# Kernel optimization log

Measured on AMD Instinct MI355X. Metric: run time of the kernel, lower is better.

Reference implementation:

```python
import jax, jax.numpy as jnp
import numpy as np

D_MODEL = 256
GAMMA = 0.9          # ret_D is built in the torch forward but never applied to the output; kept for fidelity notes
SCALE_BASE = 512     # XPOS default
TEMP = 10000.0
TWO_PI = 2.0 * np.pi


def sine_pos_embed(x):
    """DETR-style 1D sine position embedding with an all-ones mask (as in forward).
    x: [B,T,C] -> pos: [1,T,C] (mask is [1,T] ones, so batch dim broadcasts)."""
    T, C = x.shape[1], x.shape[2]
    x_embed = jnp.arange(1, T + 1, dtype=jnp.float32)          # cumsum of ones
    x_embed = x_embed / (x_embed[-1] + 1e-6) * TWO_PI          # normalize=True
    dim_t = TEMP ** (2.0 * (jnp.arange(C) // 2).astype(jnp.float32) / C)
    pos = x_embed[:, None] / dim_t                             # [T,C]
    pos = jnp.stack([jnp.sin(pos[:, 0::2]), jnp.cos(pos[:, 1::2])], axis=2).reshape(T, C)
    return pos[None].astype(x.dtype)


def _dup_interleave(m):
    # [L, d/2] -> [L, d], columns repeated pairwise: [a,b] -> [a,a,b,b]
    return jnp.repeat(m, 2, axis=-1)


def _rotate_every_two(x):
    x1, x2 = x[..., 0::2], x[..., 1::2]
    return jnp.stack([-x2, x1], axis=-1).reshape(x.shape)


def xpos_apply(x, downscale=False):
    """RetNet XPOS rotary embedding. x: [B,L,d]."""
    L, d = x.shape[1], x.shape[2]
    half = d // 2
    scale_vec = (jnp.arange(0, d, 2, dtype=jnp.float32) + 0.4 * d) / (1.4 * d)   # [d/2]
    power = jnp.arange(L, dtype=jnp.float32) / SCALE_BASE
    scale = scale_vec[None, :] ** power[:, None]                                  # [L, d/2]
    inv_freq = 1.0 / (TEMP ** (jnp.arange(half, dtype=jnp.float32) / half))
    sinusoid = jnp.arange(L, dtype=jnp.float32)[:, None] * inv_freq[None, :]      # [L, d/2]
    sin, cos = jnp.sin(sinusoid), jnp.cos(sinusoid)
    if downscale:
        scale = 1.0 / scale
    sin_s = _dup_interleave(sin * scale)[None].astype(x.dtype)   # [1,L,d]
    cos_s = _dup_interleave(cos * scale)[None].astype(x.dtype)
    return x * cos_s + _rotate_every_two(x) * sin_s


def setup_inputs() -> dict:
    key = jax.random.key(0)
    ks = jax.random.split(key, 8)
    B, TXT, VID, D = 16, 32, 2048, D_MODEL
    S = TXT + VID
    inp = {
        "src": jax.random.normal(ks[0], (B, S, D), dtype=jnp.float32),
        "learn_vid_ret": jax.random.normal(ks[1], (VID * VID, 1), dtype=jnp.float32),
        "W_txt_Q": jax.random.normal(ks[2], (D, D), dtype=jnp.float32) / D,
        "W_txt_K": jax.random.normal(ks[3], (D, D), dtype=jnp.float32) / D,
        "W_txt_V": jax.random.normal(ks[4], (D, D), dtype=jnp.float32) / D,
        "W_vid_Q": jax.random.normal(ks[5], (D, D), dtype=jnp.float32) / D,
        "W_vid_K": jax.random.normal(ks[6], (D, D), dtype=jnp.float32) / D,
        "W_vid_V": jax.random.normal(ks[7], (D, D), dtype=jnp.float32) / D,
        "txt_length": TXT,
    }
    return inp


def reference(src, learn_vid_ret, W_txt_Q, W_txt_K, W_txt_V, W_vid_Q, W_vid_K, W_vid_V, txt_length):
    S = src.shape[1]
    vid_length = S - txt_length

    # learned retention mask over the video block
    learn_ret = jax.nn.sigmoid(learn_vid_ret.reshape(vid_length, vid_length))
    diag = jnp.eye(vid_length, dtype=src.dtype)
    video_ret = (1.0 - diag) * learn_ret
    loss_sparsity = jnp.mean(jnp.abs(video_ret))

    # full [S,S] mask: ones everywhere, sigmoid(learned) on the vid-vid block
    ret_mask = jnp.ones((S, S), dtype=src.dtype).at[txt_length:, txt_length:].set(learn_ret)

    txt_mem = src[:, :txt_length]   # [B,TXT,D]
    vid_mem = src[:, txt_length:]   # [B,VID,D]

    pos = sine_pos_embed(txt_mem)   # [1,TXT,D]
    txt_Q = (pos + txt_mem) @ W_txt_Q
    txt_K = (pos + txt_mem) @ W_txt_K
    vid_Q = xpos_apply(vid_mem @ W_vid_Q)
    vid_K = xpos_apply(vid_mem @ W_vid_K, downscale=True)

    Q = jnp.concatenate([txt_Q, vid_Q], axis=1)                  # [B,S,D]
    K = jnp.concatenate([txt_K, vid_K], axis=1)                  # [B,S,D]
    V = jnp.concatenate([txt_mem @ W_txt_V, vid_mem @ W_vid_V], axis=1)

    # retention: QK^T elementwise-masked (no softmax), then weighted V sum
    scores = jnp.einsum('bsd,btd->bst', Q, K) * ret_mask[None]   # [B,S,S]
    out = scores @ V                                             # [B,S,D]
    return out, loss_sparsity
```

## Files before the change

kernel.cpp:

```cpp
#include <hip/hip_runtime.h>

#define B_   16
#define TXT  32
#define VID  2048
#define D_   256
#define S_   2080
#define SP   2176
#define NKT  34
#define GTOT 17424

typedef unsigned short ushort_t;
typedef __attribute__((ext_vector_type(8))) short short8;
typedef __attribute__((ext_vector_type(4))) short short4v;
typedef __attribute__((ext_vector_type(4))) float f32x4;
typedef __attribute__((ext_vector_type(16))) float f32x16;

__device__ __forceinline__ ushort_t f2bf(float f) {
  unsigned u = __builtin_bit_cast(unsigned, f);
  unsigned r = (u + 0x7FFFu + ((u >> 16) & 1u)) >> 16;
  return (ushort_t)r;
}
__device__ __forceinline__ float bf2f(ushort_t h) {
  unsigned u = ((unsigned)h) << 16;
  return __builtin_bit_cast(float, u);
}

__device__ __forceinline__ void g2l16(void* lds, const void* g) {
  __builtin_amdgcn_global_load_lds(
      (const __attribute__((address_space(1))) char*)g,
      (__attribute__((address_space(3))) char*)lds, 16, 0, 0);
}

__device__ __forceinline__ f32x4 mfma16(short8 a, short8 b, f32x4 c) {
  return __builtin_amdgcn_mfma_f32_16x16x32_bf16(a, b, c, 0, 0, 0);
}
__device__ __forceinline__ f32x16 mfma32(short8 a, short8 b, f32x16 c) {
  return __builtin_amdgcn_mfma_f32_32x32x16_bf16(a, b, c, 0, 0, 0);
}


__global__ void tbl_kernel(float* __restrict__ tbl) {
  int idx = blockIdx.x * 256 + threadIdx.x;
  int n = idx >> 7, i = idx & 127;
  float invf = powf(10000.0f, -(float)i / 128.0f);
  float ang = (float)n * invf;
  float s, co;
  sincosf(ang, &s, &co);
  float sv = ((float)(2 * i) + 102.4f) / 358.4f;
  float sc = powf(sv, (float)n / 512.0f);
  float4 r;
  r.x = co * sc; r.y = s * sc; r.z = co / sc; r.w = s / sc;
  *(float4*)(tbl + (size_t)idx * 4) = r;
}

__global__ void sig_loss_kernel(const float* __restrict__ learn, ushort_t* __restrict__ sigp,
                                float* __restrict__ loss) {
  const int tid = threadIdx.x;
  const int base = (blockIdx.x * 256 + tid) * 8;
  float4 v0 = *(const float4*)(learn + base);
  float4 v1 = *(const float4*)(learn + base + 4);
  float vals[8] = {v0.x, v0.y, v0.z, v0.w, v1.x, v1.y, v1.z, v1.w};
  float acc = 0.f;
  short8 sh;
  #pragma unroll
  for (int j = 0; j < 8; ++j) {
    int idx = base + j;
    float s = 1.0f / (1.0f + expf(-vals[j]));
    sh[j] = (short)f2bf(s);
    int rr = idx >> 11, cc = idx & 2047;
    if (rr != cc) acc += s;
  }
  *(short8*)(sigp + base) = sh;
  __shared__ float red[256];
  red[tid] = acc;
  __syncthreads();
  #pragma unroll
  for (int st = 128; st > 0; st >>= 1) {
    if (tid < st) red[tid] += red[tid + st];
    __syncthreads();
  }
  if (tid == 0) atomicAdd(loss, red[0] * (1.0f / 4194304.0f));
}

__global__ void cvt_kernel(const float* __restrict__ src, ushort_t* __restrict__ srcb) {
  int i = blockIdx.x * 256 + threadIdx.x;
  int b = i >> 16;
  int rem = i & 65535;
  int row = rem >> 5, c8 = (rem & 31) * 8;
  const float* p = src + ((size_t)b * S_ + TXT + row) * D_ + c8;
  float4 v0 = *(const float4*)p;
  float4 v1 = *(const float4*)(p + 4);
  short8 h;
  h[0] = (short)f2bf(v0.x); h[1] = (short)f2bf(v0.y); h[2] = (short)f2bf(v0.z); h[3] = (short)f2bf(v0.w);
  h[4] = (short)f2bf(v1.x); h[5] = (short)f2bf(v1.y); h[6] = (short)f2bf(v1.z); h[7] = (short)f2bf(v1.w);
  *(short8*)(srcb + ((size_t)b * VID + row) * D_ + c8) = h;
}

__global__ void pad0_kernel(ushort_t* __restrict__ Qp, ushort_t* __restrict__ Ks,
                            ushort_t* __restrict__ VTs) {
  int i = blockIdx.x * 256 + threadIdx.x;
  short8 z = {0, 0, 0, 0, 0, 0, 0, 0};
  if (i < 49152) {
    int bb = i / 3072, rem = i - bb * 3072;
    int row = 2080 + (rem >> 5), c8 = (rem & 31) * 8;
    *(short8*)(Qp + ((size_t)bb * SP + row) * D_ + c8) = z;
  } else if (i < 65536) {
    int j = i - 49152; int bb = j >> 10; int rem = j & 1023;
    int kstep = rem >> 6, ch = rem & 63;
    size_t base = ((size_t)(bb * NKT + 32)) << 14;
    *(short8*)(Ks + base + kstep * 1024 + 512 + ch * 8) = z;
  } else if (i < 81920) {
    int j = i - 65536; int bb = j >> 10; int rem = j & 1023;
    size_t base = (((size_t)(bb * NKT + 32)) << 14) + 8192;
    *(short8*)(VTs + base + rem * 8) = z;
  }
}

__global__ void wt_kernel(const float* __restrict__ Wq, const float* __restrict__ Wk,
                          const float* __restrict__ Wv, ushort_t* __restrict__ WT) {
  __shared__ float t[64][68];
  const int k0 = blockIdx.x * 64, n0 = blockIdx.y * 64, mt = blockIdx.z;
  const float* W = (mt == 0) ? Wq : (mt == 1) ? Wk : Wv;
  int tid = threadIdx.x;
  int r = tid >> 4, cq = (tid & 15) * 4;
  #pragma unroll
  for (int m = 0; m < 4; ++m) {
    int k = m * 16 + r;
    float4 v = *(const float4*)(W + (size_t)(k0 + k) * 256 + n0 + cq);
    t[k][cq] = v.x; t[k][cq + 1] = v.y; t[k][cq + 2] = v.z; t[k][cq + 3] = v.w;
  }
  __syncthreads();
  #pragma unroll
  for (int m = 0; m < 4; ++m) {
    int n = m * 16 + r;
    short4v h;
    h[0] = (short)f2bf(t[cq + 0][n]);
    h[1] = (short)f2bf(t[cq + 1][n]);
    h[2] = (short)f2bf(t[cq + 2][n]);
    h[3] = (short)f2bf(t[cq + 3][n]);
    *(short4v*)(WT + ((size_t)mt * D_ + n0 + n) * D_ + k0 + cq) = h;
  }
}

__global__ void txt_kernel(const float* __restrict__ src,
                           const float* __restrict__ Wq, const float* __restrict__ Wk,
                           const float* __restrict__ Wv,
                           ushort_t* __restrict__ Qp, ushort_t* __restrict__ Ks,
                           ushort_t* __restrict__ VTs) {
  __shared__ float a_s[8][256];
  __shared__ float x_s[8][256];
  const int tg = blockIdx.x;
  const int b  = blockIdx.y;
  const int c  = threadIdx.x;
  #pragma unroll
  for (int t = 0; t < 8; ++t) {
    int row = tg * 8 + t;
    float x = src[((size_t)b * S_ + row) * D_ + c];
    float xe = (float)(row + 1) * (6.283185307179586f / (32.0f + 1e-6f));
    int i = c >> 1;
    float dimt = powf(10000.0f, (2.0f * (float)i) / 256.0f);
    float ang = xe / dimt;
    float pv = (c & 1) ? cosf(ang) : sinf(ang);
    x_s[t][c] = x;
    a_s[t][c] = x + pv;
  }
  __syncthreads();
  float q[8] = {0,0,0,0,0,0,0,0}, k[8] = {0,0,0,0,0,0,0,0}, v[8] = {0,0,0,0,0,0,0,0};
  for (int kk = 0; kk < 256; ++kk) {
    float wq = Wq[(size_t)kk * 256 + c];
    float wk = Wk[(size_t)kk * 256 + c];
    float wv = Wv[(size_t)kk * 256 + c];
    #pragma unroll
    for (int t = 0; t < 8; ++t) {
      q[t] = fmaf(a_s[t][kk], wq, q[t]);
      k[t] = fmaf(a_s[t][kk], wk, k[t]);
      v[t] = fmaf(x_s[t][kk], wv, v[t]);
    }
  }
  #pragma unroll
  for (int t = 0; t < 8; ++t) {
    int row = tg * 8 + t;
    Qp[((size_t)b * SP + row) * D_ + c] = f2bf(q[t]);
    size_t kidx = ((((size_t)(b * NKT)) << 14) + (c >> 4) * 1024 + row * 16 + (c & 15)) ^ (((row >> 2) & 1) << 3);
    Ks[kidx] = f2bf(k[t]);
    size_t vidx = ((((size_t)(b * NKT)) << 14) + (row >> 4) * 4096 + c * 16 + (row & 15)) ^ (((c >> 2) & 1) << 3);
    VTs[vidx] = f2bf(v[t]);
  }
}

template <int MODE>
__global__ __launch_bounds__(256, 2) void vid_gemm(
    const float* __restrict__ src, const ushort_t* __restrict__ srcb,
    const ushort_t* __restrict__ WT, const float* __restrict__ tbl,
    ushort_t* __restrict__ Qp, ushort_t* __restrict__ Ks, ushort_t* __restrict__ VTs) {
  __shared__ __align__(16) ushort_t ldsA[64 * 64];
  __shared__ __align__(16) ushort_t ldsB[64 * 64];

  const int rt = blockIdx.x;
  const int b  = blockIdx.y;
  const int ct = blockIdx.z;
  const int nt = ct >> 2;
  const int n0 = (ct & 3) * 64;
  const int tid = threadIdx.x;
  const int wv = tid >> 6, lane = tid & 63, l15 = lane & 15, l4 = lane >> 4;

  f32x4 acc[4];
  #pragma unroll
  for (int t2 = 0; t2 < 4; ++t2) { acc[t2][0] = 0.f; acc[t2][1] = 0.f; acc[t2][2] = 0.f; acc[t2][3] = 0.f; }

  for (int kk = 0; kk < 256; kk += 64) {
    if (MODE == 1) {
      #pragma unroll
      for (int m = 0; m < 2; ++m) {
        int p = (m * 256 + tid) * 16;
        int r = p >> 7;
        int cb = (p & 127) ^ ((r & 7) << 4);
        g2l16((char*)ldsA + p,
              (const char*)(srcb + ((size_t)b * VID + rt * 64 + r) * D_ + kk) + cb);
      }
    } else {
      #pragma unroll
      for (int m = 0; m < 4; ++m) {
        int q = m * 256 + tid;
        int r = q >> 4;
        int kc = (q & 15) * 4;
        const float4 v = *(const float4*)(src + ((size_t)b * S_ + TXT + rt * 64 + r) * D_ + kk + kc);
        short4v h;
        h[0] = (short)f2bf(v.x); h[1] = (short)f2bf(v.y);
        h[2] = (short)f2bf(v.z); h[3] = (short)f2bf(v.w);
        int off = ((r << 7) + (kc << 1)) ^ ((r & 7) << 4);
        *(short4v*)((char*)ldsA + off) = h;
      }
    }
    #pragma unroll
    for (int m = 0; m < 2; ++m) {
      int p = (m * 256 + tid) * 16;
      int nl = p >> 7;
      int c = (p & 127) ^ ((nl & 7) << 4);
      g2l16((char*)ldsB + p, (const char*)(WT + ((size_t)nt * D_ + n0 + nl) * D_ + kk) + c);
    }
    __syncthreads();
    #pragma unroll
    for (int ks = 0; ks < 2; ++ks) {
      int ar = wv * 16 + l15;
      int aoff = ((ar << 7) + ((ks * 32 + l4 * 8) << 1)) ^ ((ar & 7) << 4);
      short8 av = *(const short8*)((const char*)ldsA + aoff);
      #pragma unroll
      for (int t2 = 0; t2 < 4; ++t2) {
        int nl = t2 * 16 + l15;
        int boff = ((nl << 7) + ((ks * 32 + l4 * 8) << 1)) ^ ((nl & 7) << 4);
        short8 bv = *(const short8*)((const char*)ldsB + boff);
        acc[t2] = mfma16(av, bv, acc[t2]);
      }
    }
    __syncthreads();
  }

  const int rowl = wv * 16 + l4 * 4;
  if (nt < 2) {
    #pragma unroll
    for (int t2 = 0; t2 < 4; ++t2) {
      int c = n0 + t2 * 16 + l15;
      #pragma unroll
      for (int r = 0; r < 4; ++r) {
        int n = rt * 64 + rowl + r;
        float x = acc[t2][r];
        float xp = __shfl_xor(x, 1);
        const float4 tb = *(const float4*)(tbl + ((size_t)n * 128 + (c >> 1)) * 4);
        float cs = (nt == 0) ? tb.x : tb.z;
        float ss = (nt == 0) ? tb.y : tb.w;
        float val = (c & 1) ? fmaf(x, cs, xp * ss) : fmaf(x, cs, -xp * ss);
        if (nt == 0) {
          Qp[((size_t)b * SP + TXT + n) * D_ + c] = f2bf(val);
        } else {
          int kvg = TXT + n;
          size_t kidx = ((((size_t)(b * NKT + (kvg >> 6))) << 14) + (c >> 4) * 1024 + (kvg & 63) * 16 + (c & 15))
                        ^ (((kvg >> 2) & 1) << 3);
          Ks[kidx] = f2bf(val);
        }
      }
    }
  } else {
    #pragma unroll
    for (int t2 = 0; t2 < 4; ++t2)
      #pragma unroll
      for (int r = 0; r < 4; ++r) {
        int rr = rowl + r;
        int cc = t2 * 16 + l15;
        int off = ((rr << 7) + (cc << 1)) ^ ((rr & 7) << 4);
        *(ushort_t*)((char*)ldsA + off) = f2bf(acc[t2][r]);
      }
    __syncthreads();
    int n = tid >> 2;
    int rc = (tid & 3) * 16;
    short8 o0, o1;
    #pragma unroll
    for (int j = 0; j < 8; ++j) {
      int rr = rc + j;
      int off = ((rr << 7) + (n << 1)) ^ ((rr & 7) << 4);
      o0[j] = *(const short*)((const char*)ldsA + off);
    }
    #pragma unroll
    for (int j = 0; j < 8; ++j) {
      int rr = rc + 8 + j;
      int off = ((rr << 7) + (n << 1)) ^ ((rr & 7) << 4);
      o1[j] = *(const short*)((const char*)ldsA + off);
    }
    int d = n0 + n;
    int kvg0 = TXT + rt * 64 + rc;
    size_t base = (((size_t)(b * NKT + (kvg0 >> 6))) << 14) + ((kvg0 >> 4) & 3) * 4096 + d * 16;
    int swz8 = ((d >> 2) & 1) << 3;
    *(short8*)(VTs + base + swz8) = o0;
    *(short8*)(VTs + base + (swz8 ^ 8)) = o1;
  }
}

__global__ __launch_bounds__(512, 1) void attn_kernel(
    const ushort_t* __restrict__ Qp, const ushort_t* __restrict__ Ks,
    const ushort_t* __restrict__ VTs, const ushort_t* __restrict__ sigp,
    float* __restrict__ out) {
  __shared__ __align__(16) ushort_t Kb[16384];
  __shared__ __align__(16) ushort_t Vb[16384];
  __shared__ __align__(16) ushort_t Pb[2][4096];

  const int kblk = blockIdx.x;
  const int bs = (kblk & 7) * 64 + (kblk >> 3);
  const int gs = bs * 34 + (bs >> 5);
  const int ge = (bs + 1) * 34 + ((bs + 1) >> 5);

  const int tid = threadIdx.x;
  const int wid = tid >> 6, lane = tid & 63;
  const int l31 = lane & 31, l5 = lane >> 5;
  const bool isQK = wid < 4;
  const int qh = (wid >> 1) & 1, kh = wid & 1;
  const int d0 = (wid & 3) * 64;
  const int qloc = qh * 32 + l31;

  int cb_b = gs / 1089;
  int rrem = gs - cb_b * 1089;
  int cb_q = rrem / 33;
  int cb_k = rrem - cb_q * 33;

  auto stage = [&](ushort_t* dst, const ushort_t* srcb, int bb, int tt) {
    const char* src = (const char*)srcb + (((size_t)(bb * NKT + tt)) << 15);
    #pragma unroll
    for (int m = 0; m < 4; ++m) { int s = m * 512 + tid; g2l16((char*)dst + s * 16, src + s * 16); }
  };

  short8 qf[16];
  int4 mq[4];

  auto ldq = [&](int bb, int qq) {
    const ushort_t* qrow = Qp + ((size_t)bb * SP + qq * 64 + qloc) * D_ + l5 * 8;
    #pragma unroll
    for (int ks = 0; ks < 16; ++ks) qf[ks] = *(const short8*)(qrow + ks * 16);
  };
  auto ldmask = [&](int qq, int tt) {
    int q = qq * 64 + qloc;
    int qc = q - TXT; qc = qc < 0 ? 0 : (qc > 2047 ? 2047 : qc);
    int kvp = tt * 64 + kh * 32 - TXT;
    int kvc = (kvp >= 0 && kvp <= 2016) ? kvp : 0;
    const int4* mrow = (const int4*)(sigp + (size_t)qc * 2048 + kvc);
    mq[0] = mrow[0]; mq[1] = mrow[1]; mq[2] = mrow[2]; mq[3] = mrow[3];
  };

  f32x16 oacc[2][2];
  #pragma unroll
  for (int i2 = 0; i2 < 2; ++i2)
    #pragma unroll
    for (int j2 = 0; j2 < 2; ++j2)
      #pragma unroll
      for (int r = 0; r < 16; ++r) oacc[i2][j2][r] = 0.f;

  const int kswz = ((l31 >> 2) & 1) << 4;
  const int pswz = (l31 & 7) << 4;

  if (isQK) ldmask(cb_q, cb_k);
  stage(Kb, Ks, cb_b, cb_k);
  asm volatile("s_waitcnt vmcnt(0)" ::: "memory");
  __builtin_amdgcn_sched_barrier(0);
  __builtin_amdgcn_s_barrier();
  __builtin_amdgcn_sched_barrier(0);

  int pv_b = cb_b, pv_q = cb_q, pv_k = cb_k;

  for (int i = gs; i <= ge; ++i) {
    int n1_b = cb_b, n1_q = cb_q, n1_k = cb_k;
    if (i <= ge - 2) { ++n1_k; if (n1_k == 33) { n1_k = 0; ++n1_q; if (n1_q == 33) { n1_q = 0; ++n1_b; } } }

    if (isQK) {
      if (i < ge) {
        if (cb_k == 0 || i == gs) ldq(cb_b, cb_q);
        f32x16 s0, s1;
        #pragma unroll
        for (int r = 0; r < 16; ++r) { s0[r] = 0.f; s1[r] = 0.f; }
        const int krow = (kh * 32 + l31) * 32 + l5 * 16;
        __builtin_amdgcn_s_setprio(1);
        #pragma unroll
        for (int ks = 0; ks < 8; ++ks) {
          short8 ka = *(const short8*)((const char*)Kb + ((ks * 2048 + krow) ^ kswz));
          short8 kc = *(const short8*)((const char*)Kb + (((ks + 8) * 2048 + krow) ^ kswz));
          s0 = mfma32(ka, qf[ks], s0);
          s1 = mfma32(kc, qf[ks + 8], s1);
        }
        __builtin_amdgcn_s_setprio(0);
        {
          int q = cb_q * 64 + qloc;
          bool qv = (q >= TXT) && (q < S_);
          int kvp = cb_k * 64 + kh * 32 - TXT;
          bool kvv = (kvp >= 0 && kvp <= 2016);
          bool ok = qv && kvv;
          const unsigned* mw = (const unsigned*)mq;
          #pragma unroll
          for (int t = 0; t < 4; ++t) {
            unsigned w0p, w1p;
            {
              unsigned wa = mw[4 * t + 0], wb = mw[4 * t + 2];
              unsigned w = l5 ? wb : wa;
              float m0 = ok ? bf2f((ushort_t)(w & 0xFFFFu)) : 1.0f;
              float m1 = ok ? bf2f((ushort_t)(w >> 16)) : 1.0f;
              int r = 4 * t;
              float p0 = (s0[r] + s1[r]) * m0;
              float p1 = (s0[r + 1] + s1[r + 1]) * m1;
              asm("v_cvt_pk_bf16_f32 %0, %1, %2" : "=v"(w0p) : "v"(p0), "v"(p1));
            }
            {
              unsigned wa = mw[4 * t + 1], wb = mw[4 * t + 3];
              unsigned w = l5 ? wb : wa;
              float m0 = ok ? bf2f((ushort_t)(w & 0xFFFFu)) : 1.0f;
              float m1 = ok ? bf2f((ushort_t)(w >> 16)) : 1.0f;
              int r = 4 * t + 2;
              float p0 = (s0[r] + s1[r]) * m0;
              float p1 = (s0[r + 1] + s1[r + 1]) * m1;
              asm("v_cvt_pk_bf16_f32 %0, %1, %2" : "=v"(w1p) : "v"(p0), "v"(p1));
            }
            int off = ((qloc << 7) + (kh << 6) + (t << 4) + (l5 << 3)) ^ pswz;
            *(uint2*)((char*)Pb[i & 1] + off) = make_uint2(w0p, w1p);
          }
        }
        asm volatile("s_waitcnt lgkmcnt(0)" ::: "memory");
        __builtin_amdgcn_sched_barrier(0);
      }
    } else {
      if (i > gs) {
        const int pbuf = (i & 1) ^ 1;
        __builtin_amdgcn_s_setprio(1);
        #pragma unroll
        for (int ks = 0; ks < 4; ++ks) {
          short8 pf0 = *(const short8*)((const char*)Pb[pbuf] + ((l31 * 128 + ks * 32 + l5 * 16) ^ pswz));
          short8 pf1 = *(const short8*)((const char*)Pb[pbuf] + (((32 + l31) * 128 + ks * 32 + l5 * 16) ^ pswz));
          short8 vf0 = *(const short8*)((const char*)Vb + ((ks * 8192 + (d0 + l31) * 32 + l5 * 16) ^ kswz));
          short8 vf1 = *(const short8*)((const char*)Vb + ((ks * 8192 + (d0 + 32 + l31) * 32 + l5 * 16) ^ kswz));
          oacc[0][0] = mfma32(pf0, vf0, oacc[0][0]);
          oacc[0][1] = mfma32(pf0, vf1, oacc[0][1]);
          oacc[1][0] = mfma32(pf1, vf0, oacc[1][0]);
          oacc[1][1] = mfma32(pf1, vf1, oacc[1][1]);
        }
        __builtin_amdgcn_s_setprio(0);
        asm volatile("s_waitcnt lgkmcnt(0)" ::: "memory");
        __builtin_amdgcn_sched_barrier(0);
        if (pv_k == 32 || i == ge) {
          #pragma unroll
          for (int qg2 = 0; qg2 < 2; ++qg2)
            #pragma unroll
            for (int dg = 0; dg < 2; ++dg)
              #pragma unroll
              for (int r = 0; r < 16; ++r) {
                int qg = pv_q * 64 + qg2 * 32 + (r & 3) + 8 * (r >> 2) + 4 * l5;
                int dd = d0 + dg * 32 + l31;
                if (qg < S_)
                  unsafeAtomicAdd(&out[((size_t)pv_b * S_ + qg) * D_ + dd], oacc[qg2][dg][r]);
                oacc[qg2][dg][r] = 0.f;
              }
        }
      }
    }

    __builtin_amdgcn_sched_barrier(0);
    __builtin_amdgcn_s_barrier();
    __builtin_amdgcn_sched_barrier(0);

    if (i < ge) {
      if (isQK) ldmask(n1_q, n1_k);
      stage(Kb, Ks, n1_b, n1_k);
      stage(Vb, VTs, cb_b, cb_k);
      __builtin_amdgcn_sched_barrier(0);
      if (isQK) { asm volatile("s_waitcnt vmcnt(4)" ::: "memory"); }
      else      { asm volatile("s_waitcnt vmcnt(0)" ::: "memory"); }
      __builtin_amdgcn_sched_barrier(0);
    }
    __builtin_amdgcn_s_barrier();
    __builtin_amdgcn_sched_barrier(0);

    pv_b = cb_b; pv_q = cb_q; pv_k = cb_k;
    cb_b = n1_b; cb_q = n1_q; cb_k = n1_k;
  }
}

extern "C" void kernel_launch(void* const* d_in, const int* in_sizes, int n_in,
                              void* d_out, int out_size, void* d_ws, size_t ws_size,
                              hipStream_t stream) {
  (void)in_sizes; (void)n_in;
  const float* src   = (const float*)d_in[0];
  const float* learn = (const float*)d_in[1];
  const float* Wtq = (const float*)d_in[2];
  const float* Wtk = (const float*)d_in[3];
  const float* Wtv = (const float*)d_in[4];
  const float* Wvq = (const float*)d_in[5];
  const float* Wvk = (const float*)d_in[6];
  const float* Wvv = (const float*)d_in[7];
  float* out = (float*)d_out;

  char* ws = (char*)d_ws;
  const size_t QKV_ONE  = (size_t)B_ * SP * D_ * 2;
  const size_t QP_OFF   = 0;
  const size_t KS_OFF   = QP_OFF + QKV_ONE;
  const size_t VT_OFF   = KS_OFF + QKV_ONE;
  const size_t SIG_OFF  = VT_OFF + QKV_ONE;
  const size_t TBL_OFF  = SIG_OFF + (size_t)VID * VID * 2;
  const size_t WT_OFF   = TBL_OFF + (size_t)VID * 128 * 4 * sizeof(float);
  const size_t SRCB_OFF = WT_OFF + (size_t)3 * D_ * D_ * 2;
  const size_t NEED_SRCB = SRCB_OFF + (size_t)B_ * VID * D_ * 2;

  ushort_t* Qp   = (ushort_t*)(ws + QP_OFF);
  ushort_t* Ks   = (ushort_t*)(ws + KS_OFF);
  ushort_t* VTs  = (ushort_t*)(ws + VT_OFF);
  ushort_t* sigp = (ushort_t*)(ws + SIG_OFF);
  float*    tbl  = (float*)(ws + TBL_OFF);
  ushort_t* WT   = (ushort_t*)(ws + WT_OFF);
  ushort_t* srcb = (ushort_t*)(ws + SRCB_OFF);

  hipMemsetAsync(d_out, 0, (size_t)out_size * sizeof(float), stream);
  pad0_kernel<<<320, 256, 0, stream>>>(Qp, Ks, VTs);
  tbl_kernel<<<1024, 256, 0, stream>>>(tbl);
  sig_loss_kernel<<<2048, 256, 0, stream>>>(learn, sigp, out + (size_t)B_ * S_ * D_);
  wt_kernel<<<dim3(4, 4, 3), 256, 0, stream>>>(Wvq, Wvk, Wvv, WT);
  txt_kernel<<<dim3(4, B_), 256, 0, stream>>>(src, Wtq, Wtk, Wtv, Qp, Ks, VTs);
  if (ws_size >= NEED_SRCB) {
    cvt_kernel<<<4096, 256, 0, stream>>>(src, srcb);
    vid_gemm<1><<<dim3(32, B_, 12), 256, 0, stream>>>(src, srcb, WT, tbl, Qp, Ks, VTs);
  } else {
    vid_gemm<0><<<dim3(32, B_, 12), 256, 0, stream>>>(src, srcb, WT, tbl, Qp, Ks, VTs);
  }
  attn_kernel<<<dim3(512), 512, 0, stream>>>(Qp, Ks, VTs, sigp, out);
}
```

Baseline: 352.8 us.

## Read Q/K/V fragments directly from global in tiled layout, drop LDS staging

The attention kernel no longer stages K and V tiles into shared memory with a producer/consumer warp split and double-buffered P. Each of four waves now computes QK^T directly from global memory, with Q also stored in the same 64x16-tiled layout as K, then does PV reading V fragments straight from global. The XOR swizzles are dropped and the launch changes to 1024 blocks of 256 threads. This trades LDS use and the software pipeline for more global/L2 traffic and less overlap between the QK and PV phases, while allowing higher occupancy.

```diff
diff --git a/kernel.cpp b/kernel.cpp
--- a/kernel.cpp
+++ b/kernel.cpp
@@ -96,23 +96,23 @@
   *(short8*)(srcb + ((size_t)b * VID + row) * D_ + c8) = h;
 }
 
-__global__ void pad0_kernel(ushort_t* __restrict__ Qp, ushort_t* __restrict__ Ks,
+__global__ void pad0_kernel(ushort_t* __restrict__ Qs, ushort_t* __restrict__ Ks,
                             ushort_t* __restrict__ VTs) {
   int i = blockIdx.x * 256 + threadIdx.x;
   short8 z = {0, 0, 0, 0, 0, 0, 0, 0};
-  if (i < 49152) {
-    int bb = i / 3072, rem = i - bb * 3072;
-    int row = 2080 + (rem >> 5), c8 = (rem & 31) * 8;
-    *(short8*)(Qp + ((size_t)bb * SP + row) * D_ + c8) = z;
-  } else if (i < 65536) {
-    int j = i - 49152; int bb = j >> 10; int rem = j & 1023;
+  int sec = i >> 14;
+  int j = i & 16383;
+  int bb = j >> 10;
+  int rem = j & 1023;
+  size_t base = ((size_t)(bb * NKT + 32)) << 14;
+  if (sec == 0) {
     int kstep = rem >> 6, ch = rem & 63;
-    size_t base = ((size_t)(bb * NKT + 32)) << 14;
+    *(short8*)(Qs + base + kstep * 1024 + 512 + ch * 8) = z;
+  } else if (sec == 1) {
+    int kstep = rem >> 6, ch = rem & 63;
     *(short8*)(Ks + base + kstep * 1024 + 512 + ch * 8) = z;
-  } else if (i < 81920) {
-    int j = i - 65536; int bb = j >> 10; int rem = j & 1023;
-    size_t base = (((size_t)(bb * NKT + 32)) << 14) + 8192;
-    *(short8*)(VTs + base + rem * 8) = z;
+  } else {
+    *(short8*)(VTs + base + 8192 + rem * 8) = z;
   }
 }
 
@@ -145,7 +145,7 @@
 __global__ void txt_kernel(const float* __restrict__ src,
                            const float* __restrict__ Wq, const float* __restrict__ Wk,
                            const float* __restrict__ Wv,
-                           ushort_t* __restrict__ Qp, ushort_t* __restrict__ Ks,
+                           ushort_t* __restrict__ Qs, ushort_t* __restrict__ Ks,
                            ushort_t* __restrict__ VTs) {
   __shared__ float a_s[8][256];
   __shared__ float x_s[8][256];
@@ -180,11 +180,11 @@
   #pragma unroll
   for (int t = 0; t < 8; ++t) {
     int row = tg * 8 + t;
-    Qp[((size_t)b * SP + row) * D_ + c] = f2bf(q[t]);
-    size_t kidx = ((((size_t)(b * NKT)) << 14) + (c >> 4) * 1024 + row * 16 + (c & 15)) ^ (((row >> 2) & 1) << 3);
-    Ks[kidx] = f2bf(k[t]);
-    size_t vidx = ((((size_t)(b * NKT)) << 14) + (row >> 4) * 4096 + c * 16 + (row & 15)) ^ (((c >> 2) & 1) << 3);
-    VTs[vidx] = f2bf(v[t]);
+    size_t base = ((size_t)(b * NKT)) << 14;
+    size_t sub = (size_t)(c >> 4) * 1024 + row * 16 + (c & 15);
+    Qs[base + sub] = f2bf(q[t]);
+    Ks[base + sub] = f2bf(k[t]);
+    VTs[base + (size_t)(row >> 4) * 4096 + c * 16 + (row & 15)] = f2bf(v[t]);
   }
 }
 
@@ -192,7 +192,7 @@
 __global__ __launch_bounds__(256, 2) void vid_gemm(
     const float* __restrict__ src, const ushort_t* __restrict__ srcb,
     const ushort_t* __restrict__ WT, const float* __restrict__ tbl,
-    ushort_t* __restrict__ Qp, ushort_t* __restrict__ Ks, ushort_t* __restrict__ VTs) {
+    ushort_t* __restrict__ Qs, ushort_t* __restrict__ Ks, ushort_t* __restrict__ VTs) {
   __shared__ __align__(16) ushort_t ldsA[64 * 64];
   __shared__ __align__(16) ushort_t ldsB[64 * 64];
 
@@ -270,14 +270,11 @@
         float cs = (nt == 0) ? tb.x : tb.z;
         float ss = (nt == 0) ? tb.y : tb.w;
         float val = (c & 1) ? fmaf(x, cs, xp * ss) : fmaf(x, cs, -xp * ss);
-        if (nt == 0) {
-          Qp[((size_t)b * SP + TXT + n) * D_ + c] = f2bf(val);
-        } else {
-          int kvg = TXT + n;
-          size_t kidx = ((((size_t)(b * NKT + (kvg >> 6))) << 14) + (c >> 4) * 1024 + (kvg & 63) * 16 + (c & 15))
-                        ^ (((kvg >> 2) & 1) << 3);
-          Ks[kidx] = f2bf(val);
-        }
+        int rowg = TXT + n;
+        size_t idx = (((size_t)(b * NKT + (rowg >> 6))) << 14)
+                   + (size_t)(c >> 4) * 1024 + (rowg & 63) * 16 + (c & 15);
+        if (nt == 0) Qs[idx] = f2bf(val);
+        else         Ks[idx] = f2bf(val);
       }
     }
   } else {
@@ -309,60 +306,31 @@
     int d = n0 + n;
     int kvg0 = TXT + rt * 64 + rc;
     size_t base = (((size_t)(b * NKT + (kvg0 >> 6))) << 14) + ((kvg0 >> 4) & 3) * 4096 + d * 16;
-    int swz8 = ((d >> 2) & 1) << 3;
-    *(short8*)(VTs + base + swz8) = o0;
-    *(short8*)(VTs + base + (swz8 ^ 8)) = o1;
-  }
-}
-
-__global__ __launch_bounds__(512, 1) void attn_kernel(
-    const ushort_t* __restrict__ Qp, const ushort_t* __restrict__ Ks,
+    *(short8*)(VTs + base) = o0;
+    *(short8*)(VTs + base + 8) = o1;
+  }
+}
+
+__global__ __launch_bounds__(256) void attn_kernel(
+    const ushort_t* __restrict__ Qs, const ushort_t* __restrict__ Ks,
     const ushort_t* __restrict__ VTs, const ushort_t* __restrict__ sigp,
     float* __restrict__ out) {
-  __shared__ __align__(16) ushort_t Kb[16384];
-  __shared__ __align__(16) ushort_t Vb[16384];
-  __shared__ __align__(16) ushort_t Pb[2][4096];
+  __shared__ __align__(16) ushort_t Pb[4096];
 
   const int kblk = blockIdx.x;
-  const int bs = (kblk & 7) * 64 + (kblk >> 3);
-  const int gs = bs * 34 + (bs >> 5);
-  const int ge = (bs + 1) * 34 + ((bs + 1) >> 5);
+  const int bs = (kblk & 7) * 128 + (kblk >> 3);
+  int g = bs * 17 + (bs >> 6);
+  const int gend = (bs + 1) * 17 + ((bs + 1) >> 6);
 
   const int tid = threadIdx.x;
   const int wid = tid >> 6, lane = tid & 63;
   const int l31 = lane & 31, l5 = lane >> 5;
-  const bool isQK = wid < 4;
-  const int qh = (wid >> 1) & 1, kh = wid & 1;
-  const int d0 = (wid & 3) * 64;
+  const int qh = wid >> 1, kh = wid & 1;
+  const int d0 = wid * 64;
   const int qloc = qh * 32 + l31;
-
-  int cb_b = gs / 1089;
-  int rrem = gs - cb_b * 1089;
-  int cb_q = rrem / 33;
-  int cb_k = rrem - cb_q * 33;
-
-  auto stage = [&](ushort_t* dst, const ushort_t* srcb, int bb, int tt) {
-    const char* src = (const char*)srcb + (((size_t)(bb * NKT + tt)) << 15);
-    #pragma unroll
-    for (int m = 0; m < 4; ++m) { int s = m * 512 + tid; g2l16((char*)dst + s * 16, src + s * 16); }
-  };
-
-  short8 qf[16];
-  int4 mq[4];
-
-  auto ldq = [&](int bb, int qq) {
-    const ushort_t* qrow = Qp + ((size_t)bb * SP + qq * 64 + qloc) * D_ + l5 * 8;
-    #pragma unroll
-    for (int ks = 0; ks < 16; ++ks) qf[ks] = *(const short8*)(qrow + ks * 16);
-  };
-  auto ldmask = [&](int qq, int tt) {
-    int q = qq * 64 + qloc;
-    int qc = q - TXT; qc = qc < 0 ? 0 : (qc > 2047 ? 2047 : qc);
-    int kvp = tt * 64 + kh * 32 - TXT;
-    int kvc = (kvp >= 0 && kvp <= 2016) ? kvp : 0;
-    const int4* mrow = (const int4*)(sigp + (size_t)qc * 2048 + kvc);
-    mq[0] = mrow[0]; mq[1] = mrow[1]; mq[2] = mrow[2]; mq[3] = mrow[3];
-  };
+  const int pswz = (l31 & 7) << 4;
+
+  int b = g / 1089, rem = g - b * 1089, qt = rem / 33, kvt = rem - qt * 33;
 
   f32x16 oacc[2][2];
   #pragma unroll
@@ -372,128 +340,109 @@
       #pragma unroll
       for (int r = 0; r < 16; ++r) oacc[i2][j2][r] = 0.f;
 
-  const int kswz = ((l31 >> 2) & 1) << 4;
-  const int pswz = (l31 & 7) << 4;
-
-  if (isQK) ldmask(cb_q, cb_k);
-  stage(Kb, Ks, cb_b, cb_k);
-  asm volatile("s_waitcnt vmcnt(0)" ::: "memory");
-  __builtin_amdgcn_sched_barrier(0);
-  __builtin_amdgcn_s_barrier();
-  __builtin_amdgcn_sched_barrier(0);
-
-  int pv_b = cb_b, pv_q = cb_q, pv_k = cb_k;
-
-  for (int i = gs; i <= ge; ++i) {
-    int n1_b = cb_b, n1_q = cb_q, n1_k = cb_k;
-    if (i <= ge - 2) { ++n1_k; if (n1_k == 33) { n1_k = 0; ++n1_q; if (n1_q == 33) { n1_q = 0; ++n1_b; } } }
-
-    if (isQK) {
-      if (i < ge) {
-        if (cb_k == 0 || i == gs) ldq(cb_b, cb_q);
-        f32x16 s0, s1;
-        #pragma unroll
-        for (int r = 0; r < 16; ++r) { s0[r] = 0.f; s1[r] = 0.f; }
-        const int krow = (kh * 32 + l31) * 32 + l5 * 16;
-        __builtin_amdgcn_s_setprio(1);
-        #pragma unroll
-        for (int ks = 0; ks < 8; ++ks) {
-          short8 ka = *(const short8*)((const char*)Kb + ((ks * 2048 + krow) ^ kswz));
-          short8 kc = *(const short8*)((const char*)Kb + (((ks + 8) * 2048 + krow) ^ kswz));
-          s0 = mfma32(ka, qf[ks], s0);
-          s1 = mfma32(kc, qf[ks + 8], s1);
+  while (g < gend) {
+    int4 mq[4];
+    {
+      int q = qt * 64 + qloc;
+      int qc = q - TXT; qc = qc < 0 ? 0 : (qc > 2047 ? 2047 : qc);
+      int kvp = kvt * 64 + kh * 32 - TXT;
+      int kvc = (kvp >= 0 && kvp <= 2016) ? kvp : 0;
+      const int4* mrow = (const int4*)(sigp + (size_t)qc * 2048 + kvc);
+      mq[0] = mrow[0]; mq[1] = mrow[1]; mq[2] = mrow[2]; mq[3] = mrow[3];
+    }
+
+    const ushort_t* kb = Ks + (((size_t)(b * NKT + kvt)) << 14) + (kh * 32 + l31) * 16 + l5 * 8;
+    const ushort_t* qb = Qs + (((size_t)(b * NKT + qt)) << 14) + qloc * 16 + l5 * 8;
+    f32x16 s;
+    #pragma unroll
+    for (int r = 0; r < 16; ++r) s[r] = 0.f;
+    __builtin_amdgcn_s_setprio(1);
+    #pragma unroll
+    for (int ks = 0; ks < 16; ++ks) {
+      short8 kf = *(const short8*)(kb + ks * 1024);
+      short8 qf = *(const short8*)(qb + ks * 1024);
+      s = mfma32(kf, qf, s);
+    }
+    __builtin_amdgcn_s_setprio(0);
+
+    {
+      int q = qt * 64 + qloc;
+      bool qv = (q >= TXT) && (q < S_);
+      int kvp = kvt * 64 + kh * 32 - TXT;
+      bool kvv = (kvp >= 0 && kvp <= 2016);
+      bool ok = qv && kvv;
+      const unsigned* mw = (const unsigned*)mq;
+      #pragma unroll
+      for (int t = 0; t < 4; ++t) {
+        unsigned w0p, w1p;
+        {
+          unsigned wa = mw[4 * t + 0], wb = mw[4 * t + 2];
+          unsigned w = l5 ? wb : wa;
+          float m0 = ok ? bf2f((ushort_t)(w & 0xFFFFu)) : 1.0f;
+          float m1 = ok ? bf2f((ushort_t)(w >> 16)) : 1.0f;
+          int r = 4 * t;
+          float p0 = s[r] * m0;
+          float p1 = s[r + 1] * m1;
+          asm("v_cvt_pk_bf16_f32 %0, %1, %2" : "=v"(w0p) : "v"(p0), "v"(p1));
         }
-        __builtin_amdgcn_s_setprio(0);
         {
-          int q = cb_q * 64 + qloc;
-          bool qv = (q >= TXT) && (q < S_);
-          int kvp = cb_k * 64 + kh * 32 - TXT;
-          bool kvv = (kvp >= 0 && kvp <= 2016);
-          bool ok = qv && kvv;
-          const unsigned* mw = (const unsigned*)mq;
-          #pragma unroll
-          for (int t = 0; t < 4; ++t) {
-            unsigned w0p, w1p;
-            {
-              unsigned wa = mw[4 * t + 0], wb = mw[4 * t + 2];
-              unsigned w = l5 ? wb : wa;
-              float m0 = ok ? bf2f((ushort_t)(w & 0xFFFFu)) : 1.0f;
-              float m1 = ok ? bf2f((ushort_t)(w >> 16)) : 1.0f;
-              int r = 4 * t;
-              float p0 = (s0[r] + s1[r]) * m0;
-              float p1 = (s0[r + 1] + s1[r + 1]) * m1;
-              asm("v_cvt_pk_bf16_f32 %0, %1, %2" : "=v"(w0p) : "v"(p0), "v"(p1));
-            }
-            {
-              unsigned wa = mw[4 * t + 1], wb = mw[4 * t + 3];
-              unsigned w = l5 ? wb : wa;
-              float m0 = ok ? bf2f((ushort_t)(w & 0xFFFFu)) : 1.0f;
-              float m1 = ok ? bf2f((ushort_t)(w >> 16)) : 1.0f;
-              int r = 4 * t + 2;
-              float p0 = (s0[r] + s1[r]) * m0;
-              float p1 = (s0[r + 1] + s1[r + 1]) * m1;
-              asm("v_cvt_pk_bf16_f32 %0, %1, %2" : "=v"(w1p) : "v"(p0), "v"(p1));
-            }
-            int off = ((qloc << 7) + (kh << 6) + (t << 4) + (l5 << 3)) ^ pswz;
-            *(uint2*)((char*)Pb[i & 1] + off) = make_uint2(w0p, w1p);
-          }
+          unsigned wa = mw[4 * t + 1], wb = mw[4 * t + 3];
+          unsigned w = l5 ? wb : wa;
+          float m0 = ok ? bf2f((ushort_t)(w & 0xFFFFu)) : 1.0f;
+          float m1 = ok ? bf2f((ushort_t)(w >> 16)) : 1.0f;
+          int r = 4 * t + 2;
+          float p0 = s[r] * m0;
+          float p1 = s[r + 1] * m1;
+          asm("v_cvt_pk_bf16_f32 %0, %1, %2" : "=v"(w1p) : "v"(p0), "v"(p1));
         }
-        asm volatile("s_waitcnt lgkmcnt(0)" ::: "memory");
-        __builtin_amdgcn_sched_barrier(0);
-      }
-    } else {
-      if (i > gs) {
-        const int pbuf = (i & 1) ^ 1;
-        __builtin_amdgcn_s_setprio(1);
-        #pragma unroll
-        for (int ks = 0; ks < 4; ++ks) {
-          short8 pf0 = *(const short8*)((const char*)Pb[pbuf] + ((l31 * 128 + ks * 32 + l5 * 16) ^ pswz));
-          short8 pf1 = *(const short8*)((const char*)Pb[pbuf] + (((32 + l31) * 128 + ks * 32 + l5 * 16) ^ pswz));
-          short8 vf0 = *(const short8*)((const char*)Vb + ((ks * 8192 + (d0 + l31) * 32 + l5 * 16) ^ kswz));
-          short8 vf1 = *(const short8*)((const char*)Vb + ((ks * 8192 + (d0 + 32 + l31) * 32 + l5 * 16) ^ kswz));
-          oacc[0][0] = mfma32(pf0, vf0, oacc[0][0]);
-          oacc[0][1] = mfma32(pf0, vf1, oacc[0][1]);
-          oacc[1][0] = mfma32(pf1, vf0, oacc[1][0]);
-          oacc[1][1] = mfma32(pf1, vf1, oacc[1][1]);
-        }
-        __builtin_amdgcn_s_setprio(0);
-        asm volatile("s_waitcnt lgkmcnt(0)" ::: "memory");
-        __builtin_amdgcn_sched_barrier(0);
-        if (pv_k == 32 || i == ge) {
-          #pragma unroll
-          for (int qg2 = 0; qg2 < 2; ++qg2)
-            #pragma unroll
-            for (int dg = 0; dg < 2; ++dg)
-              #pragma unroll
-              for (int r = 0; r < 16; ++r) {
-                int qg = pv_q * 64 + qg2 * 32 + (r & 3) + 8 * (r >> 2) + 4 * l5;
-                int dd = d0 + dg * 32 + l31;
-                if (qg < S_)
-                  unsafeAtomicAdd(&out[((size_t)pv_b * S_ + qg) * D_ + dd], oacc[qg2][dg][r]);
-                oacc[qg2][dg][r] = 0.f;
-              }
-        }
-      }
-    }
-
+        int off = ((qloc << 7) + (kh << 6) + (t << 4) + (l5 << 3)) ^ pswz;
+        *(uint2*)((char*)Pb + off) = make_uint2(w0p, w1p);
+      }
+    }
+
+    asm volatile("s_waitcnt lgkmcnt(0)" ::: "memory");
     __builtin_amdgcn_sched_barrier(0);
     __builtin_amdgcn_s_barrier();
     __builtin_amdgcn_sched_barrier(0);
 
-    if (i < ge) {
-      if (isQK) ldmask(n1_q, n1_k);
-      stage(Kb, Ks, n1_b, n1_k);
-      stage(Vb, VTs, cb_b, cb_k);
-      __builtin_amdgcn_sched_barrier(0);
-      if (isQK) { asm volatile("s_waitcnt vmcnt(4)" ::: "memory"); }
-      else      { asm volatile("s_waitcnt vmcnt(0)" ::: "memory"); }
-      __builtin_amdgcn_sched_barrier(0);
-    }
+    const ushort_t* vb = VTs + (((size_t)(b * NKT + kvt)) << 14) + (size_t)d0 * 16 + l5 * 8;
+    __builtin_amdgcn_s_setprio(1);
+    #pragma unroll
+    for (int ks = 0; ks < 4; ++ks) {
+      short8 pf0 = *(const short8*)((const char*)Pb + ((l31 * 128 + ks * 32 + l5 * 16) ^ pswz));
+      short8 pf1 = *(const short8*)((const char*)Pb + (((32 + l31) * 128 + ks * 32 + l5 * 16) ^ pswz));
+      short8 vf0 = *(const short8*)(vb + ks * 4096 + l31 * 16);
+      short8 vf1 = *(const short8*)(vb + ks * 4096 + (l31 + 32) * 16);
+      oacc[0][0] = mfma32(pf0, vf0, oacc[0][0]);
+      oacc[0][1] = mfma32(pf0, vf1, oacc[0][1]);
+      oacc[1][0] = mfma32(pf1, vf0, oacc[1][0]);
+      oacc[1][1] = mfma32(pf1, vf1, oacc[1][1]);
+    }
+    __builtin_amdgcn_s_setprio(0);
+    asm volatile("s_waitcnt lgkmcnt(0)" ::: "memory");
+    __builtin_amdgcn_sched_barrier(0);
+
+    if (kvt == 32 || g + 1 == gend) {
+      #pragma unroll
+      for (int qg2 = 0; qg2 < 2; ++qg2)
+        #pragma unroll
+        for (int dg = 0; dg < 2; ++dg)
+          #pragma unroll
+          for (int r = 0; r < 16; ++r) {
+            int qg = qt * 64 + qg2 * 32 + (r & 3) + 8 * (r >> 2) + 4 * l5;
+            int dd = d0 + dg * 32 + l31;
+            if (qg < S_)
+              unsafeAtomicAdd(&out[((size_t)b * S_ + qg) * D_ + dd], oacc[qg2][dg][r]);
+            oacc[qg2][dg][r] = 0.f;
+          }
+    }
+
     __builtin_amdgcn_s_barrier();
     __builtin_amdgcn_sched_barrier(0);
 
-    pv_b = cb_b; pv_q = cb_q; pv_k = cb_k;
-    cb_b = n1_b; cb_q = n1_q; cb_k = n1_k;
+    ++g;
+    ++kvt;
+    if (kvt == 33) { kvt = 0; ++qt; if (qt == 33) { qt = 0; ++b; } }
   }
 }
 
@@ -522,7 +471,7 @@
   const size_t SRCB_OFF = WT_OFF + (size_t)3 * D_ * D_ * 2;
   const size_t NEED_SRCB = SRCB_OFF + (size_t)B_ * VID * D_ * 2;
 
-  ushort_t* Qp   = (ushort_t*)(ws + QP_OFF);
+  ushort_t* Qs   = (ushort_t*)(ws + QP_OFF);
   ushort_t* Ks   = (ushort_t*)(ws + KS_OFF);
   ushort_t* VTs  = (ushort_t*)(ws + VT_OFF);
   ushort_t* sigp = (ushort_t*)(ws + SIG_OFF);
@@ -531,16 +480,16 @@
   ushort_t* srcb = (ushort_t*)(ws + SRCB_OFF);
 
   hipMemsetAsync(d_out, 0, (size_t)out_size * sizeof(float), stream);
-  pad0_kernel<<<320, 256, 0, stream>>>(Qp, Ks, VTs);
+  pad0_kernel<<<192, 256, 0, stream>>>(Qs, Ks, VTs);
   tbl_kernel<<<1024, 256, 0, stream>>>(tbl);
   sig_loss_kernel<<<2048, 256, 0, stream>>>(learn, sigp, out + (size_t)B_ * S_ * D_);
   wt_kernel<<<dim3(4, 4, 3), 256, 0, stream>>>(Wvq, Wvk, Wvv, WT);
-  txt_kernel<<<dim3(4, B_), 256, 0, stream>>>(src, Wtq, Wtk, Wtv, Qp, Ks, VTs);
+  txt_kernel<<<dim3(4, B_), 256, 0, stream>>>(src, Wtq, Wtk, Wtv, Qs, Ks, VTs);
   if (ws_size >= NEED_SRCB) {
     cvt_kernel<<<4096, 256, 0, stream>>>(src, srcb);
-    vid_gemm<1><<<dim3(32, B_, 12), 256, 0, stream>>>(src, srcb, WT, tbl, Qp, Ks, VTs);
+    vid_gemm<1><<<dim3(32, B_, 12), 256, 0, stream>>>(src, srcb, WT, tbl, Qs, Ks, VTs);
   } else {
-    vid_gemm<0><<<dim3(32, B_, 12), 256, 0, stream>>>(src, srcb, WT, tbl, Qp, Ks, VTs);
-  }
-  attn_kernel<<<dim3(512), 512, 0, stream>>>(Qp, Ks, VTs, sigp, out);
-}
+    vid_gemm<0><<<dim3(32, B_, 12), 256, 0, stream>>>(src, srcb, WT, tbl, Qs, Ks, VTs);
+  }
+  attn_kernel<<<dim3(1024), 256, 0, stream>>>(Qs, Ks, VTs, sigp, out);
+}
```

After: 356.8 us. Within noise of the previous version (+1.1%).
